# Optimization experiments

Hardware: AMD Instinct MI355X
Metric: run time of the kernel (lower is better)

Reference implementation:

```python
import jax, jax.numpy as jnp
import numpy as np

EPS = 1e-3  # BatchNorm1d eps


def _fc_relu(x, W, b):
    return jax.nn.relu(x @ W + b)


def _fc_bn_relu(x, W, b, gamma, beta):
    # Linear -> BatchNorm1d (training mode: batch stats, biased var) -> ReLU
    h = x @ W + b
    m = jnp.mean(h, axis=0)
    v = jnp.var(h, axis=0)  # biased, matches torch BN normalization
    return jax.nn.relu((h - m) * jax.lax.rsqrt(v + EPS) * gamma + beta)


def _mmnet(img, tag, lat, lon, Wi, bi, gi, bti, Wt, bt, gt, btt, Wl, bl, gl, btl,
           W1, b1, W2, b2, W3, b3, W4, b4, W5, b5, W6, b6, W7, b7):
    img = _fc_bn_relu(img, Wi, bi, gi, bti)          # [B,300]
    tag = _fc_bn_relu(tag, Wt, bt, gt, btt)          # [B,300]
    loc = jnp.concatenate([lat, lon], axis=1)        # [B,2]
    loc = _fc_bn_relu(loc, Wl, bl, gl, btl)          # [B,10]
    x = jnp.concatenate([loc, img, tag], axis=1)     # [B,610]
    x = _fc_relu(x, W1, b1)                          # [B,2048]
    x = _fc_relu(x, W2, b2)                          # [B,2048]
    x = _fc_relu(x, W3, b3)                          # [B,1024]
    x = _fc_relu(x, W4, b4)                          # [B,1024]
    x = _fc_relu(x, W5, b5)                          # [B,512]
    x = _fc_relu(x, W6, b6)                          # [B,512]
    return x @ W7 + b7                               # [B,1]


def setup_inputs() -> dict:
    key = jax.random.key(0)
    ks = iter(jax.random.split(key, 64))
    B = 16384
    inp = {}
    inp['img_p'] = jax.random.normal(next(ks), (B, 300), jnp.float32)
    inp['tag_p'] = jax.random.normal(next(ks), (B, 300), jnp.float32)
    inp['lat_p'] = jax.random.uniform(next(ks), (B, 1), jnp.float32)
    inp['lon_p'] = jax.random.uniform(next(ks), (B, 1), jnp.float32)
    inp['img_n'] = jax.random.normal(next(ks), (B, 300), jnp.float32)
    inp['tag_n'] = jax.random.normal(next(ks), (B, 300), jnp.float32)
    inp['lat_n'] = jax.random.uniform(next(ks), (B, 1), jnp.float32)
    inp['lon_n'] = jax.random.uniform(next(ks), (B, 1), jnp.float32)
    inp['margin'] = 1

    def lin(din, dout):
        # matches l.weight.data.normal_(0, 0.01), bias zero; stored [din,dout]
        return (jax.random.normal(next(ks), (din, dout), jnp.float32) * 0.01,
                jnp.zeros((dout,), jnp.float32))

    inp['Wi'], inp['bi'] = lin(300, 300)
    inp['gi'], inp['bti'] = jnp.ones((300,), jnp.float32), jnp.zeros((300,), jnp.float32)
    inp['Wt'], inp['bt'] = lin(300, 300)
    inp['gt'], inp['btt'] = jnp.ones((300,), jnp.float32), jnp.zeros((300,), jnp.float32)
    inp['Wl'], inp['bl'] = lin(2, 10)
    inp['gl'], inp['btl'] = jnp.ones((10,), jnp.float32), jnp.zeros((10,), jnp.float32)
    inp['W1'], inp['b1'] = lin(610, 2048)
    inp['W2'], inp['b2'] = lin(2048, 2048)
    inp['W3'], inp['b3'] = lin(2048, 1024)
    inp['W4'], inp['b4'] = lin(1024, 1024)
    inp['W5'], inp['b5'] = lin(1024, 512)
    inp['W6'], inp['b6'] = lin(512, 512)
    inp['W7'], inp['b7'] = lin(512, 1)
    return inp


def reference(img_p, tag_p, lat_p, lon_p, img_n, tag_n, lat_n, lon_n,
              Wi, bi, gi, bti, Wt, bt, gt, btt, Wl, bl, gl, btl,
              W1, b1, W2, b2, W3, b3, W4, b4, W5, b5, W6, b6, W7, b7, margin):
    params = (Wi, bi, gi, bti, Wt, bt, gt, btt, Wl, bl, gl, btl,
              W1, b1, W2, b2, W3, b3, W4, b4, W5, b5, W6, b6, W7, b7)
    score_p = _mmnet(img_p, tag_p, lat_p, lon_p, *params)  # [B,1]
    score_n = _mmnet(img_n, tag_n, lat_n, lon_n, *params)  # [B,1]
    # vectorized replacement of the per-element python loop
    correct = jnp.sum((score_p - score_n)[:, 0] > margin).astype(jnp.int32)
    return score_p, score_n, correct
```

## Files before the change

kernel.cpp:

```cpp
#include <hip/hip_runtime.h>
#include <hip/hip_fp16.h>

typedef _Float16 half8 __attribute__((ext_vector_type(8)));
typedef float f32x16 __attribute__((ext_vector_type(16)));

#define B_ROWS 16384
#define M_ALL  32768

__device__ __forceinline__ void glds16(void* lds, const void* g) {
  __builtin_amdgcn_global_load_lds(
      (const __attribute__((address_space(1))) unsigned int*)g,
      (__attribute__((address_space(3))) unsigned int*)lds, 16, 0, 0);
}

template<int EPI>
__global__ __launch_bounds__(256, 2)
void gemm128(const _Float16* __restrict__ A, const _Float16* __restrict__ Bt,
             const float* __restrict__ bias, _Float16* __restrict__ Cout,
             int M, int N, int K) {
  __shared__ _Float16 As[128 * 64];
  __shared__ _Float16 Bs[128 * 64];
  const int tid = threadIdx.x;
  const int w = tid >> 6, l = tid & 63;
  const int bm = blockIdx.y << 7, bn = blockIdx.x << 7;
  const int wm = (w >> 1) << 6, wn = (w & 1) << 6;
  const int l31 = l & 31, g5 = l >> 5, l7 = l & 7, l3 = l >> 3;

  f32x16 acc[2][2];
#pragma unroll
  for (int i = 0; i < 2; ++i)
#pragma unroll
    for (int j = 0; j < 2; ++j)
#pragma unroll
      for (int r = 0; r < 16; ++r) acc[i][j][r] = 0.f;

  const int schunk = (l7 ^ l3) * 8;
  const int srow = w * 32 + l3;

  for (int kt = 0; kt < K; kt += 64) {
#pragma unroll
    for (int c = 0; c < 4; ++c)
      glds16(&As[w * 2048 + c * 512],
             A + (size_t)(bm + srow + c * 8) * K + kt + schunk);
#pragma unroll
    for (int c = 0; c < 4; ++c)
      glds16(&Bs[w * 2048 + c * 512],
             Bt + (size_t)(bn + srow + c * 8) * K + kt + schunk);
    __syncthreads();
#pragma unroll
    for (int ks = 0; ks < 4; ++ks) {
      const int p0 = (((ks * 2 + g5) ^ l7)) * 8;
      half8 af[2], bf[2];
#pragma unroll
      for (int i = 0; i < 2; ++i)
        af[i] = *(const half8*)&As[(wm + i * 32 + l31) * 64 + p0];
#pragma unroll
      for (int i = 0; i < 2; ++i)
        bf[i] = *(const half8*)&Bs[(wn + i * 32 + l31) * 64 + p0];
#pragma unroll
      for (int i = 0; i < 2; ++i)
#pragma unroll
        for (int j = 0; j < 2; ++j)
          acc[i][j] = __builtin_amdgcn_mfma_f32_32x32x16_f16(af[i], bf[j], acc[i][j], 0, 0, 0);
    }
    __syncthreads();
  }

#pragma unroll
  for (int i = 0; i < 2; ++i)
#pragma unroll
    for (int j = 0; j < 2; ++j) {
      const int col = bn + wn + j * 32 + l31;
      float bv = 0.f;
      if (EPI == 1) bv = bias[col];
#pragma unroll
      for (int r = 0; r < 16; ++r) {
        const int row = bm + wm + i * 32 + (r & 3) + 8 * (r >> 2) + 4 * g5;
        const float v = acc[i][j][r] + bv;
        Cout[(size_t)row * N + col] = (_Float16)(EPI == 1 ? fmaxf(v, 0.f) : v);
      }
    }
}

__global__ __launch_bounds__(512, 1)
void gemm256(const _Float16* __restrict__ A, const _Float16* __restrict__ Bt,
             const float* __restrict__ bias, _Float16* __restrict__ Cout,
             int M, int N, int K) {
  __shared__ _Float16 smem[4 * 256 * 64];
  const int tid = threadIdx.x;
  const int w = tid >> 6, l = tid & 63;
  const int bm = blockIdx.y << 8, bn = blockIdx.x << 8;
  const int wm = w >> 2, wn = w & 3;
  const int l31 = l & 31, g5 = l >> 5, l7 = l & 7, l3 = l >> 3;

  f32x16 acc[4][2];
#pragma unroll
  for (int i = 0; i < 4; ++i)
#pragma unroll
    for (int j = 0; j < 2; ++j)
#pragma unroll
      for (int r = 0; r < 16; ++r) acc[i][j][r] = 0.f;

  const int schunk = (l7 ^ l3) * 8;
  const _Float16* aSrc = A + (size_t)(bm + w * 32 + l3) * K + schunk;
  const _Float16* bSrc = Bt + (size_t)(bn + w * 32 + l3) * K + schunk;
  const int NT = K >> 6;

  auto stage = [&](int buf, int t) {
    _Float16* as = smem + buf * 16384;
    _Float16* bs = smem + 32768 + buf * 16384;
    const size_t ko = (size_t)t * 64;
#pragma unroll
    for (int c = 0; c < 4; ++c)
      glds16(as + (w * 32 + c * 8) * 64, aSrc + (size_t)c * 8 * K + ko);
#pragma unroll
    for (int c = 0; c < 4; ++c)
      glds16(bs + (w * 32 + c * 8) * 64, bSrc + (size_t)c * 8 * K + ko);
  };

  stage(0, 0);
  stage(1, 1);
  asm volatile("s_waitcnt vmcnt(8)" ::: "memory");
  __builtin_amdgcn_s_barrier();

  half8 bf[2][4];
  for (int t = 0; t < NT; ++t) {
    const _Float16* as = smem + (t & 1) * 16384;
    const _Float16* bs = smem + 32768 + (t & 1) * 16384;
#pragma unroll
    for (int p = 0; p < 4; ++p) {
      half8 af[2][4];
#pragma unroll
      for (int i = 0; i < 2; ++i)
#pragma unroll
        for (int ks = 0; ks < 4; ++ks)
          af[i][ks] = *(const half8*)(as + (wm * 128 + (p * 2 + i) * 32 + l31) * 64
                                         + ((ks * 2 + g5) ^ l7) * 8);
      if (p == 0) {
#pragma unroll
        for (int j = 0; j < 2; ++j)
#pragma unroll
          for (int ks = 0; ks < 4; ++ks)
            bf[j][ks] = *(const half8*)(bs + (wn * 64 + j * 32 + l31) * 64
                                           + ((ks * 2 + g5) ^ l7) * 8);
      }
      __builtin_amdgcn_s_barrier();
      asm volatile("s_waitcnt lgkmcnt(0)" ::: "memory");
      __builtin_amdgcn_sched_barrier(0);
      __builtin_amdgcn_s_setprio(1);
#pragma unroll
      for (int ks = 0; ks < 4; ++ks)
#pragma unroll
        for (int i = 0; i < 2; ++i)
#pragma unroll
          for (int j = 0; j < 2; ++j)
            acc[p * 2 + i][j] = __builtin_amdgcn_mfma_f32_32x32x16_f16(
                af[i][ks], bf[j][ks], acc[p * 2 + i][j], 0, 0, 0);
      __builtin_amdgcn_s_setprio(0);
      if (p < 3) __builtin_amdgcn_s_barrier();
    }
    asm volatile("s_waitcnt vmcnt(0)" ::: "memory");
    __builtin_amdgcn_s_barrier();
    if (t + 2 < NT) stage(t & 1, t + 2);
  }

#pragma unroll
  for (int mi = 0; mi < 4; ++mi)
#pragma unroll
    for (int nj = 0; nj < 2; ++nj) {
      const int col = bn + wn * 64 + nj * 32 + l31;
      const float bv = bias[col];
#pragma unroll
      for (int r = 0; r < 16; ++r) {
        const int row = bm + wm * 128 + mi * 32 + (r & 3) + 8 * (r >> 2) + 4 * g5;
        Cout[(size_t)row * N + col] = (_Float16)fmaxf(acc[mi][nj][r] + bv, 0.f);
      }
    }
}

__global__ void tpose_pad(const float* __restrict__ src, _Float16* __restrict__ dst,
                          int Ks, int Ns, int Kd, int Nd) {
  __shared__ float t[32][33];
  const int k0 = blockIdx.x * 32, n0 = blockIdx.y * 32;
  const int tx = threadIdx.x & 31, ty = threadIdx.x >> 5;
#pragma unroll
  for (int i = ty; i < 32; i += 8) {
    const int k = k0 + i, n = n0 + tx;
    t[i][tx] = (k < Ks && n < Ns) ? src[(size_t)k * Ns + n] : 0.f;
  }
  __syncthreads();
#pragma unroll
  for (int i = ty; i < 32; i += 8)
    dst[(size_t)(n0 + i) * Kd + (k0 + tx)] = (_Float16)t[tx][i];
}

__global__ void cvt_in_k(const float* __restrict__ xp, const float* __restrict__ xn,
                         _Float16* __restrict__ X, int C, int Cp) {
  const size_t total = (size_t)M_ALL * Cp;
  const size_t stride = (size_t)gridDim.x * blockDim.x;
  for (size_t idx = (size_t)blockIdx.x * blockDim.x + threadIdx.x; idx < total; idx += stride) {
    const int r = (int)(idx / Cp);
    const int c = (int)(idx - (size_t)r * Cp);
    float v = 0.f;
    if (c < C) v = (r < B_ROWS) ? xp[(size_t)r * C + c] : xn[(size_t)(r - B_ROWS) * C + c];
    X[idx] = (_Float16)v;
  }
}

__global__ void stats_k(const _Float16* __restrict__ h, float* __restrict__ sums, int ldh, int C) {
  const int half = blockIdx.y;
  const int nr = B_ROWS / gridDim.x;
  const int r0 = half * B_ROWS + blockIdx.x * nr;
  for (int c = threadIdx.x; c < C; c += blockDim.x) {
    float s = 0.f, q = 0.f;
    for (int r = 0; r < nr; ++r) {
      const float v = (float)h[(size_t)(r0 + r) * ldh + c];
      s += v; q += v * v;
    }
    atomicAdd(&sums[(half * 2 + 0) * 384 + c], s);
    atomicAdd(&sums[(half * 2 + 1) * 384 + c], q);
  }
}

__global__ void bn_apply_k(const _Float16* __restrict__ h, const float* __restrict__ sums,
                           const float* __restrict__ gamma, const float* __restrict__ beta,
                           _Float16* __restrict__ X1, int coff) {
  const size_t total = (size_t)M_ALL * 300;
  const size_t stride = (size_t)gridDim.x * blockDim.x;
  for (size_t idx = (size_t)blockIdx.x * blockDim.x + threadIdx.x; idx < total; idx += stride) {
    const int r = (int)(idx / 300);
    const int c = (int)(idx - (size_t)r * 300);
    const int hf = r >> 14;
    const float mean = sums[(hf * 2 + 0) * 384 + c] * (1.f / 16384.f);
    const float ms   = sums[(hf * 2 + 1) * 384 + c] * (1.f / 16384.f);
    const float inv = rsqrtf(ms - mean * mean + 1e-3f) * gamma[c];
    const float y = ((float)h[(size_t)r * 384 + c] - mean) * inv + beta[c];
    X1[(size_t)r * 640 + coff + c] = (_Float16)fmaxf(y, 0.f);
  }
}

__global__ void loc_k(const float* __restrict__ lat_p, const float* __restrict__ lon_p,
                      const float* __restrict__ lat_n, const float* __restrict__ lon_n,
                      const float* __restrict__ Wl, const float* __restrict__ gl,
                      const float* __restrict__ btl, _Float16* __restrict__ X1) {
  const int j = blockIdx.x, half = blockIdx.y;
  const float* lat = half ? lat_n : lat_p;
  const float* lon = half ? lon_n : lon_p;
  const float w0 = Wl[j], w1 = Wl[10 + j];
  const int t = threadIdx.x;
  float s = 0.f, q = 0.f;
  for (int r = t; r < B_ROWS; r += 256) {
    const float v = lat[r] * w0 + lon[r] * w1;
    s += v; q += v * v;
  }
  __shared__ float rs[256], rq[256];
  rs[t] = s; rq[t] = q;
  __syncthreads();
  for (int o = 128; o; o >>= 1) {
    if (t < o) { rs[t] += rs[t + o]; rq[t] += rq[t + o]; }
    __syncthreads();
  }
  const float mean = rs[0] * (1.f / 16384.f);
  const float var = rq[0] * (1.f / 16384.f) - mean * mean;
  const float inv = rsqrtf(var + 1e-3f) * gl[j];
  const float bb = btl[j];
  for (int r = t; r < B_ROWS; r += 256) {
    const float v = lat[r] * w0 + lon[r] * w1;
    const float y = (v - mean) * inv + bb;
    X1[(size_t)(half * B_ROWS + r) * 640 + j] = (_Float16)fmaxf(y, 0.f);
  }
}

__global__ void scores_k(const _Float16* __restrict__ Y, const float* __restrict__ w7,
                         const float* __restrict__ b7, float* __restrict__ out) {
  const int row = blockIdx.x * 4 + (threadIdx.x >> 6);
  const int l = threadIdx.x & 63;
  const half8 v = *(const half8*)(Y + (size_t)row * 512 + l * 8);
  float s = 0.f;
#pragma unroll
  for (int j = 0; j < 8; ++j) s += (float)v[j] * w7[l * 8 + j];
#pragma unroll
  for (int o = 32; o; o >>= 1) s += __shfl_down(s, o);
  if (l == 0) out[row] = s + b7[0];
}

__global__ void correct_k(const float* __restrict__ sc, const int* __restrict__ mg,
                          float* __restrict__ dst) {
  __shared__ int red[256];
  const int t = threadIdx.x;
  const float m = (float)(*mg);
  int c = 0;
  for (int i = t; i < B_ROWS; i += 256)
    c += (sc[i] - sc[B_ROWS + i]) > m ? 1 : 0;
  red[t] = c;
  __syncthreads();
  for (int o = 128; o; o >>= 1) {
    if (t < o) red[t] += red[t + o];
    __syncthreads();
  }
  if (t == 0) dst[0] = (float)red[0];
}

extern "C" void kernel_launch(void* const* d_in, const int* in_sizes, int n_in,
                              void* d_out, int out_size, void* d_ws, size_t ws_size,
                              hipStream_t stream) {
  const float* img_p = (const float*)d_in[0];
  const float* tag_p = (const float*)d_in[1];
  const float* lat_p = (const float*)d_in[2];
  const float* lon_p = (const float*)d_in[3];
  const float* img_n = (const float*)d_in[4];
  const float* tag_n = (const float*)d_in[5];
  const float* lat_n = (const float*)d_in[6];
  const float* lon_n = (const float*)d_in[7];
  const int*   margin = (const int*)d_in[8];
  const float* Wi = (const float*)d_in[9];
  const float* gi = (const float*)d_in[11];
  const float* bti = (const float*)d_in[12];
  const float* Wt = (const float*)d_in[13];
  const float* gt = (const float*)d_in[15];
  const float* btt = (const float*)d_in[16];
  const float* Wl = (const float*)d_in[17];
  const float* gl = (const float*)d_in[19];
  const float* btl = (const float*)d_in[20];
  const float* W1 = (const float*)d_in[21]; const float* b1 = (const float*)d_in[22];
  const float* W2 = (const float*)d_in[23]; const float* b2 = (const float*)d_in[24];
  const float* W3 = (const float*)d_in[25]; const float* b3 = (const float*)d_in[26];
  const float* W4 = (const float*)d_in[27]; const float* b4 = (const float*)d_in[28];
  const float* W5 = (const float*)d_in[29]; const float* b5 = (const float*)d_in[30];
  const float* W6 = (const float*)d_in[31]; const float* b6 = (const float*)d_in[32];
  const float* W7 = (const float*)d_in[33]; const float* b7 = (const float*)d_in[34];
  float* out = (float*)d_out;

  char* ws = (char*)d_ws;
  size_t off = 0;
  auto alloc = [&](size_t bytes) -> void* {
    void* p = ws + off;
    off += (bytes + 255) & ~(size_t)255;
    return p;
  };
  _Float16* WiT = (_Float16*)alloc((size_t)384 * 320 * 2);
  _Float16* WtT = (_Float16*)alloc((size_t)384 * 320 * 2);
  _Float16* W1T = (_Float16*)alloc((size_t)2048 * 640 * 2);
  _Float16* W2T = (_Float16*)alloc((size_t)2048 * 2048 * 2);
  _Float16* W3T = (_Float16*)alloc((size_t)1024 * 2048 * 2);
  _Float16* W4T = (_Float16*)alloc((size_t)1024 * 1024 * 2);
  _Float16* W5T = (_Float16*)alloc((size_t)512 * 1024 * 2);
  _Float16* W6T = (_Float16*)alloc((size_t)512 * 512 * 2);
  float* sbuf = (float*)alloc((size_t)2 * 4 * 384 * 4);
  _Float16* X1 = (_Float16*)alloc((size_t)M_ALL * 640 * 2);

  const size_t persist = off;
  const size_t avail = ws_size > persist ? ws_size - persist : 0;
  int CR = 4096;
  if (avail >= (size_t)2 * 32768 * 2048 * 2) CR = 32768;
  else if (avail >= (size_t)2 * 16384 * 2048 * 2) CR = 16384;
  else if (avail >= (size_t)2 * 8192 * 2048 * 2) CR = 8192;
  _Float16* Ya = (_Float16*)(ws + persist);
  _Float16* Yb = Ya + (size_t)CR * 2048;
  _Float16* Ximg = Ya;
  _Float16* hbuf = (_Float16*)((char*)Ya + (size_t)M_ALL * 320 * 2);

  (void)hipMemsetAsync(X1, 0, (size_t)M_ALL * 640 * 2, stream);
  (void)hipMemsetAsync(sbuf, 0, (size_t)2 * 4 * 384 * 4, stream);

  tpose_pad<<<dim3(10, 12), 256, 0, stream>>>(Wi, WiT, 300, 300, 320, 384);
  tpose_pad<<<dim3(10, 12), 256, 0, stream>>>(Wt, WtT, 300, 300, 320, 384);
  tpose_pad<<<dim3(20, 64), 256, 0, stream>>>(W1, W1T, 610, 2048, 640, 2048);
  tpose_pad<<<dim3(64, 64), 256, 0, stream>>>(W2, W2T, 2048, 2048, 2048, 2048);
  tpose_pad<<<dim3(64, 32), 256, 0, stream>>>(W3, W3T, 2048, 1024, 2048, 1024);
  tpose_pad<<<dim3(32, 32), 256, 0, stream>>>(W4, W4T, 1024, 1024, 1024, 1024);
  tpose_pad<<<dim3(32, 16), 256, 0, stream>>>(W5, W5T, 1024, 512, 1024, 512);
  tpose_pad<<<dim3(16, 16), 256, 0, stream>>>(W6, W6T, 512, 512, 512, 512);

  cvt_in_k<<<2048, 256, 0, stream>>>(img_p, img_n, Ximg, 300, 320);
  gemm128<2><<<dim3(3, 256), 256, 0, stream>>>(Ximg, WiT, nullptr, hbuf, M_ALL, 384, 320);
  stats_k<<<dim3(128, 2), 256, 0, stream>>>(hbuf, sbuf, 384, 300);
  bn_apply_k<<<2048, 256, 0, stream>>>(hbuf, sbuf, gi, bti, X1, 10);
  cvt_in_k<<<2048, 256, 0, stream>>>(tag_p, tag_n, Ximg, 300, 320);
  gemm128<2><<<dim3(3, 256), 256, 0, stream>>>(Ximg, WtT, nullptr, hbuf, M_ALL, 384, 320);
  stats_k<<<dim3(128, 2), 256, 0, stream>>>(hbuf, sbuf + 4 * 384, 384, 300);
  bn_apply_k<<<2048, 256, 0, stream>>>(hbuf, sbuf + 4 * 384, gt, btt, X1, 310);
  loc_k<<<dim3(10, 2), 256, 0, stream>>>(lat_p, lon_p, lat_n, lon_n, Wl, gl, btl, X1);

  for (int c0 = 0; c0 < M_ALL; c0 += CR) {
    const int rb = CR / 128, rb2 = CR / 256;
    const _Float16* Xc = X1 + (size_t)c0 * 640;
    gemm256<<<dim3(8, rb2), 512, 0, stream>>>(Xc, W1T, b1, Ya, CR, 2048, 640);
    gemm256<<<dim3(8, rb2), 512, 0, stream>>>(Ya, W2T, b2, Yb, CR, 2048, 2048);
    gemm256<<<dim3(4, rb2), 512, 0, stream>>>(Yb, W3T, b3, Ya, CR, 1024, 2048);
    gemm256<<<dim3(4, rb2), 512, 0, stream>>>(Ya, W4T, b4, Yb, CR, 1024, 1024);
    gemm128<1><<<dim3(4, rb), 256, 0, stream>>>(Yb, W5T, b5, Ya, CR, 512, 1024);
    gemm128<1><<<dim3(4, rb), 256, 0, stream>>>(Ya, W6T, b6, Yb, CR, 512, 512);
    scores_k<<<CR / 4, 256, 0, stream>>>(Yb, W7, b7, out + c0);
  }

  correct_k<<<1, 256, 0, stream>>>(out, margin, out + 32768);
}
```

Measured before the change: 1.035 ms.

## Remove per-phase barriers in gemm256 and remap workgroups for L2 locality

Within gemm256, the inner K-tile loop no longer uses four phases separated by workgroup barriers and sched_barriers. It now loads half of the A fragments plus the B fragments, then the other half of A, and issues the MFMAs in two groups, so the compiler can overlap LDS reads with matrix math. Workgroup IDs are also remapped in a strided pattern (orig&7 times nwg/8 plus orig>>3) to change the order in which tiles are scheduled, aiming for better cache reuse. Holding all the fragments at once raises register pressure, and the remap assumes the workgroup count is divisible by 8.

```diff
diff --git a/kernel.cpp b/kernel.cpp
--- a/kernel.cpp
+++ b/kernel.cpp
@@ -89,7 +89,11 @@
   __shared__ _Float16 smem[4 * 256 * 64];
   const int tid = threadIdx.x;
   const int w = tid >> 6, l = tid & 63;
-  const int bm = blockIdx.y << 8, bn = blockIdx.x << 8;
+  const int nwg = gridDim.x * gridDim.y;
+  const int orig = blockIdx.y * gridDim.x + blockIdx.x;
+  const int wgid = (orig & 7) * (nwg >> 3) + (orig >> 3);
+  const int bx = wgid % gridDim.x, by = wgid / gridDim.x;
+  const int bm = by << 8, bn = bx << 8;
   const int wm = w >> 2, wn = w & 3;
   const int l31 = l & 31, g5 = l >> 5, l7 = l & 7, l3 = l >> 3;
 
@@ -123,42 +127,46 @@
   asm volatile("s_waitcnt vmcnt(8)" ::: "memory");
   __builtin_amdgcn_s_barrier();
 
-  half8 bf[2][4];
   for (int t = 0; t < NT; ++t) {
     const _Float16* as = smem + (t & 1) * 16384;
     const _Float16* bs = smem + 32768 + (t & 1) * 16384;
-#pragma unroll
-    for (int p = 0; p < 4; ++p) {
-      half8 af[2][4];
+    half8 af0[2][4], af1[2][4], bf[2][4];
+#pragma unroll
+    for (int i = 0; i < 2; ++i)
+#pragma unroll
+      for (int ks = 0; ks < 4; ++ks)
+        af0[i][ks] = *(const half8*)(as + (wm * 128 + i * 32 + l31) * 64
+                                        + ((ks * 2 + g5) ^ l7) * 8);
+#pragma unroll
+    for (int j = 0; j < 2; ++j)
+#pragma unroll
+      for (int ks = 0; ks < 4; ++ks)
+        bf[j][ks] = *(const half8*)(bs + (wn * 64 + j * 32 + l31) * 64
+                                       + ((ks * 2 + g5) ^ l7) * 8);
+#pragma unroll
+    for (int i = 0; i < 2; ++i)
+#pragma unroll
+      for (int ks = 0; ks < 4; ++ks)
+        af1[i][ks] = *(const half8*)(as + (wm * 128 + (2 + i) * 32 + l31) * 64
+                                        + ((ks * 2 + g5) ^ l7) * 8);
+    __builtin_amdgcn_s_setprio(1);
+#pragma unroll
+    for (int ks = 0; ks < 4; ++ks)
 #pragma unroll
       for (int i = 0; i < 2; ++i)
 #pragma unroll
-        for (int ks = 0; ks < 4; ++ks)
-          af[i][ks] = *(const half8*)(as + (wm * 128 + (p * 2 + i) * 32 + l31) * 64
-                                         + ((ks * 2 + g5) ^ l7) * 8);
-      if (p == 0) {
-#pragma unroll
         for (int j = 0; j < 2; ++j)
-#pragma unroll
-          for (int ks = 0; ks < 4; ++ks)
-            bf[j][ks] = *(const half8*)(bs + (wn * 64 + j * 32 + l31) * 64
-                                           + ((ks * 2 + g5) ^ l7) * 8);
-      }
-      __builtin_amdgcn_s_barrier();
-      asm volatile("s_waitcnt lgkmcnt(0)" ::: "memory");
-      __builtin_amdgcn_sched_barrier(0);
-      __builtin_amdgcn_s_setprio(1);
-#pragma unroll
-      for (int ks = 0; ks < 4; ++ks)
-#pragma unroll
-        for (int i = 0; i < 2; ++i)
-#pragma unroll
-          for (int j = 0; j < 2; ++j)
-            acc[p * 2 + i][j] = __builtin_amdgcn_mfma_f32_32x32x16_f16(
-                af[i][ks], bf[j][ks], acc[p * 2 + i][j], 0, 0, 0);
-      __builtin_amdgcn_s_setprio(0);
-      if (p < 3) __builtin_amdgcn_s_barrier();
-    }
+          acc[i][j] = __builtin_amdgcn_mfma_f32_32x32x16_f16(
+              af0[i][ks], bf[j][ks], acc[i][j], 0, 0, 0);
+#pragma unroll
+    for (int ks = 0; ks < 4; ++ks)
+#pragma unroll
+      for (int i = 0; i < 2; ++i)
+#pragma unroll
+        for (int j = 0; j < 2; ++j)
+          acc[2 + i][j] = __builtin_amdgcn_mfma_f32_32x32x16_f16(
+              af1[i][ks], bf[j][ks], acc[2 + i][j], 0, 0, 0);
+    __builtin_amdgcn_s_setprio(0);
     asm volatile("s_waitcnt vmcnt(0)" ::: "memory");
     __builtin_amdgcn_s_barrier();
     if (t + 2 < NT) stage(t & 1, t + 2);
```

New measurement: 970.1 us. 6.3% less time.
